# Kernel tuning notes

Measured on AMD Instinct MI355X. Metric: run time of the kernel, lower is better.

Reference implementation:

```python
import jax, jax.numpy as jnp
import numpy as np

N_NODES = 100000
N_EDGES = 1600000
IN_DIM, HIDDEN, OUT = 128, 64, 32


def setup_inputs() -> dict:
    key = jax.random.key(0)
    k1, k2, k3, k4 = jax.random.split(key, 4)
    x = jax.random.normal(k1, (N_NODES, IN_DIM), dtype=jnp.float32)
    edge_index = jax.random.randint(k2, (2, N_EDGES), 0, N_NODES, dtype=jnp.int64)
    # Glorot-style init for GCN weights
    W1 = jax.random.normal(k3, (IN_DIM, HIDDEN), dtype=jnp.float32) / np.sqrt(IN_DIM)
    b1 = jnp.zeros((HIDDEN,), dtype=jnp.float32)
    W2 = jax.random.normal(k4, (HIDDEN, OUT), dtype=jnp.float32) / np.sqrt(HIDDEN)
    b2 = jnp.zeros((OUT,), dtype=jnp.float32)
    return {"x": x, "edge_index": edge_index, "W1": W1, "b1": b1, "W2": W2, "b2": b2}


def _gcn_conv(x, src, dst, W, b, n_nodes):
    """PyG GCNConv: h = W x; symmetric-normalized scatter-add over edges
    (self-loops already appended to src/dst)."""
    h = x @ W  # [N, F_out] — transform first (F_out <= F_in)
    ones = jnp.ones_like(dst, dtype=h.dtype)
    deg = jax.ops.segment_sum(ones, dst, num_segments=n_nodes)  # in-degree incl. self-loop
    dinv = jnp.where(deg > 0, jax.lax.rsqrt(deg), 0.0)
    norm = dinv[src] * dinv[dst]  # [E]
    msg = h[src] * norm[:, None]  # [E, F_out] — dominant gather
    agg = jax.ops.segment_sum(msg, dst, num_segments=n_nodes)  # [N, F_out]
    return agg + b


def reference(x, edge_index, W1, b1, W2, b2):
    n_nodes = x.shape[0]
    loops = jnp.arange(n_nodes, dtype=edge_index.dtype)
    src = jnp.concatenate([edge_index[0], loops])
    dst = jnp.concatenate([edge_index[1], loops])
    h = jax.nn.relu(_gcn_conv(x, src, dst, W1, b1, n_nodes))
    out = jax.nn.relu(_gcn_conv(h, src, dst, W2, b2, n_nodes))
    return out
```

## Files before the change

### kernel.cpp

```cpp
#include <hip/hip_runtime.h>

#define IN_DIM 128
#define HID    64
#define OUTD   32

#define BSHIFT 9
#define BNODES 512
#define NB     196
#define BCAP   16384
#define CHUNK  4096

#define XPAD   136

typedef __attribute__((ext_vector_type(8))) short bf16x8;
typedef __attribute__((ext_vector_type(4))) float f32x4;


__device__ __forceinline__ unsigned bfp2(float x, float y) {
    unsigned a = __float_as_uint(x); a = a + 0x7FFF + ((a >> 16) & 1);
    unsigned b = __float_as_uint(y); b = b + 0x7FFF + ((b >> 16) & 1);
    return (a >> 16) | (b & 0xFFFF0000u);
}

__device__ __forceinline__ unsigned short bf1(float x) {
    unsigned u = __float_as_uint(x);
    u += 0x7FFF + ((u >> 16) & 1);
    return (unsigned short)(u >> 16);
}

__device__ __forceinline__ void acc8(float* f, uint4 q) {
    f[0] += __uint_as_float(q.x << 16); f[1] += __uint_as_float(q.x & 0xFFFF0000u);
    f[2] += __uint_as_float(q.y << 16); f[3] += __uint_as_float(q.y & 0xFFFF0000u);
    f[4] += __uint_as_float(q.z << 16); f[5] += __uint_as_float(q.z & 0xFFFF0000u);
    f[6] += __uint_as_float(q.w << 16); f[7] += __uint_as_float(q.w & 0xFFFF0000u);
}

__device__ __forceinline__ void facc8(float* f, uint4 q, float s) {
    f[0] = fmaf(__uint_as_float(q.x << 16),          s, f[0]);
    f[1] = fmaf(__uint_as_float(q.x & 0xFFFF0000u),  s, f[1]);
    f[2] = fmaf(__uint_as_float(q.y << 16),          s, f[2]);
    f[3] = fmaf(__uint_as_float(q.y & 0xFFFF0000u),  s, f[3]);
    f[4] = fmaf(__uint_as_float(q.z << 16),          s, f[4]);
    f[5] = fmaf(__uint_as_float(q.z & 0xFFFF0000u),  s, f[5]);
    f[6] = fmaf(__uint_as_float(q.w << 16),          s, f[6]);
    f[7] = fmaf(__uint_as_float(q.w & 0xFFFF0000u),  s, f[7]);
}


__launch_bounds__(256)
__global__ void k_bsct(const int* __restrict__ src, const int* __restrict__ dst,
                       int* __restrict__ bucketCursor, int* __restrict__ ebuf, int E) {
    __shared__ int h[NB];
    __shared__ int lbase[NB];
    __shared__ int lcur[NB];
    const int t = threadIdx.x;
    const int base = blockIdx.x * CHUNK;
    const int nI4 = (min(CHUNK, E - base)) >> 2;
    const int4* d4 = (const int4*)(dst + base);
    const int4* s4 = (const int4*)(src + base);

    int4 dv0, dv1, dv2, dv3;
    const bool v0 = t < nI4, v1 = t + 256 < nI4, v2 = t + 512 < nI4, v3 = t + 768 < nI4;
    if (v0) dv0 = d4[t];
    if (v1) dv1 = d4[t + 256];
    if (v2) dv2 = d4[t + 512];
    if (v3) dv3 = d4[t + 768];

    for (int i = t; i < NB; i += 256) { h[i] = 0; lcur[i] = 0; }
    __syncthreads();

    if (v0) { atomicAdd(&h[dv0.x >> BSHIFT], 1); atomicAdd(&h[dv0.y >> BSHIFT], 1);
              atomicAdd(&h[dv0.z >> BSHIFT], 1); atomicAdd(&h[dv0.w >> BSHIFT], 1); }
    if (v1) { atomicAdd(&h[dv1.x >> BSHIFT], 1); atomicAdd(&h[dv1.y >> BSHIFT], 1);
              atomicAdd(&h[dv1.z >> BSHIFT], 1); atomicAdd(&h[dv1.w >> BSHIFT], 1); }
    if (v2) { atomicAdd(&h[dv2.x >> BSHIFT], 1); atomicAdd(&h[dv2.y >> BSHIFT], 1);
              atomicAdd(&h[dv2.z >> BSHIFT], 1); atomicAdd(&h[dv2.w >> BSHIFT], 1); }
    if (v3) { atomicAdd(&h[dv3.x >> BSHIFT], 1); atomicAdd(&h[dv3.y >> BSHIFT], 1);
              atomicAdd(&h[dv3.z >> BSHIFT], 1); atomicAdd(&h[dv3.w >> BSHIFT], 1); }
    __syncthreads();

    for (int i = t; i < NB; i += 256)
        lbase[i] = h[i] ? atomicAdd(&bucketCursor[i], h[i]) : 0;
    __syncthreads();

    #define SC1(D, S) { int b_ = (D) >> BSHIFT; int off_ = atomicAdd(&lcur[b_], 1); \
                        ebuf[(size_t)b_ * BCAP + lbase[b_] + off_] = ((S) << BSHIFT) | ((D) & (BNODES - 1)); }
    if (v0) { int4 sv = s4[t];       SC1(dv0.x, sv.x); SC1(dv0.y, sv.y); SC1(dv0.z, sv.z); SC1(dv0.w, sv.w); }
    if (v1) { int4 sv = s4[t + 256]; SC1(dv1.x, sv.x); SC1(dv1.y, sv.y); SC1(dv1.z, sv.z); SC1(dv1.w, sv.w); }
    if (v2) { int4 sv = s4[t + 512]; SC1(dv2.x, sv.x); SC1(dv2.y, sv.y); SC1(dv2.z, sv.z); SC1(dv2.w, sv.w); }
    if (v3) { int4 sv = s4[t + 768]; SC1(dv3.x, sv.x); SC1(dv3.y, sv.y); SC1(dv3.z, sv.z); SC1(dv3.w, sv.w); }
    #undef SC1
}


__launch_bounds__(256)
__global__ void k_bfg(const int* __restrict__ ebuf, const int* __restrict__ bucketCursor,
                      int* __restrict__ rs, int* __restrict__ re, float* __restrict__ dinv,
                      int* __restrict__ csr,
                      const float* __restrict__ x, const float* __restrict__ W1,
                      unsigned short* __restrict__ hs1b, int N) {
    __shared__ int hist[BNODES];
    __shared__ int rsl[BNODES];
    __shared__ int ssum[256];
    __shared__ unsigned short xsb[64 * XPAD];
    __shared__ unsigned short wsb[64 * XPAD];
    const int t = threadIdx.x;

    if ((int)blockIdx.x < NB) {
        const int b = blockIdx.x;
        const int nodeBase = b << BSHIFT;
        const int ebase = b * BCAP;
        const int cnt = bucketCursor[b];
        const int nI4 = cnt >> 2;
        const int4* e4 = (const int4*)(ebuf + ebase);

        hist[t] = 0; hist[t + 256] = 0;
        __syncthreads();
        for (int i = t; i < nI4; i += 256) {
            int4 v = e4[i];
            atomicAdd(&hist[v.x & (BNODES - 1)], 1);
            atomicAdd(&hist[v.y & (BNODES - 1)], 1);
            atomicAdd(&hist[v.z & (BNODES - 1)], 1);
            atomicAdd(&hist[v.w & (BNODES - 1)], 1);
        }
        if (t < (cnt & 3))
            atomicAdd(&hist[ebuf[ebase + (nI4 << 2) + t] & (BNODES - 1)], 1);
        __syncthreads();

        int h0 = hist[2 * t], h1 = hist[2 * t + 1];
        ssum[t] = h0 + h1;
        __syncthreads();
        for (int off = 1; off < 256; off <<= 1) {
            int u = (t >= off) ? ssum[t - off] : 0;
            __syncthreads();
            ssum[t] += u;
            __syncthreads();
        }
        int excl = ssum[t] - h0 - h1;
        rsl[2 * t]     = excl;
        rsl[2 * t + 1] = excl + h0;

        int n0 = nodeBase + 2 * t, n1 = n0 + 1;
        if (n0 < N) {
            rs[n0] = ebase + excl;           re[n0] = ebase + excl + h0;
            dinv[n0] = rsqrtf((float)h0 + 1.0f);
        }
        if (n1 < N) {
            rs[n1] = ebase + excl + h0;      re[n1] = ebase + excl + h0 + h1;
            dinv[n1] = rsqrtf((float)h1 + 1.0f);
        }

        hist[2 * t] = 0; hist[2 * t + 1] = 0;
        __syncthreads();

        #define FILL1(P) { int l_ = (P) & (BNODES - 1); int off_ = atomicAdd(&hist[l_], 1); \
                           csr[ebase + rsl[l_] + off_] = ((unsigned)(P)) >> BSHIFT; }
        for (int i = t; i < nI4; i += 256) {
            int4 v = e4[i];
            FILL1(v.x); FILL1(v.y); FILL1(v.z); FILL1(v.w);
        }
        if (t < (cnt & 3))
            FILL1(ebuf[ebase + (nI4 << 2) + t]);
        #undef FILL1
    } else {
        const int base = ((int)blockIdx.x - NB) * 64;

        for (int i = t; i < IN_DIM * HID; i += 256) {
            int k = i >> 6, n = i & 63;
            wsb[n * XPAD + k] = bf1(W1[i]);
        }
        {
            const float4* s4 = (const float4*)(x + (size_t)base * IN_DIM);
            #pragma unroll
            for (int j = 0; j < 8; ++j) {
                int idx = t + j * 256;
                int r = idx >> 5, k4 = (idx & 31) * 4;
                ushort4 o;
                if (base + r < N) {
                    float4 v = s4[idx];
                    o.x = bf1(v.x); o.y = bf1(v.y); o.z = bf1(v.z); o.w = bf1(v.w);
                } else {
                    o.x = 0; o.y = 0; o.z = 0; o.w = 0;
                }
                *(ushort4*)&xsb[r * XPAD + k4] = o;
            }
        }
        __syncthreads();

        const int lane = t & 63;
        const int w    = t >> 6;
        const int lr   = lane & 15;
        const int kg   = lane >> 4;

        f32x4 acc0 = {0,0,0,0}, acc1 = {0,0,0,0}, acc2 = {0,0,0,0}, acc3 = {0,0,0,0};
        #pragma unroll
        for (int kb = 0; kb < 4; ++kb) {
            int ko = kb * 32 + kg * 8;
            bf16x8 af = *(const bf16x8*)&xsb[(w * 16 + lr) * XPAD + ko];
            bf16x8 b0 = *(const bf16x8*)&wsb[( 0 + lr) * XPAD + ko];
            bf16x8 b1 = *(const bf16x8*)&wsb[(16 + lr) * XPAD + ko];
            bf16x8 b2 = *(const bf16x8*)&wsb[(32 + lr) * XPAD + ko];
            bf16x8 b3 = *(const bf16x8*)&wsb[(48 + lr) * XPAD + ko];
            acc0 = __builtin_amdgcn_mfma_f32_16x16x32_bf16(af, b0, acc0, 0, 0, 0);
            acc1 = __builtin_amdgcn_mfma_f32_16x16x32_bf16(af, b1, acc1, 0, 0, 0);
            acc2 = __builtin_amdgcn_mfma_f32_16x16x32_bf16(af, b2, acc2, 0, 0, 0);
            acc3 = __builtin_amdgcn_mfma_f32_16x16x32_bf16(af, b3, acc3, 0, 0, 0);
        }

        #pragma unroll
        for (int j = 0; j < 4; ++j) {
            int node = base + w * 16 + kg * 4 + j;
            if (node < N) {
                unsigned short* o = hs1b + (size_t)node * HID + lr;
                o[0]  = bf1(acc0[j]);
                o[16] = bf1(acc1[j]);
                o[32] = bf1(acc2[j]);
                o[48] = bf1(acc3[j]);
            }
        }
    }
}


__launch_bounds__(128)
__global__ void k_fuse2(const uint4* __restrict__ hs, const int* __restrict__ rs,
                        const int* __restrict__ re, const int* __restrict__ csr,
                        const float* __restrict__ dinv,
                        const float* __restrict__ b1, const float* __restrict__ W2,
                        uint2* __restrict__ hs2b, int N) {
    __shared__ float Ws[HID * OUTD];
    __shared__ float L1s[16 * 68];
    const int t = threadIdx.x;
    const int base = blockIdx.x * 16;

    for (int i = t; i < HID * OUTD / 4; i += 128)
        ((float4*)Ws)[i] = ((const float4*)W2)[i];

    {
        int node = base + (t >> 3);
        int lane = t & 7;
        float dn = dinv[node];
        float fa[8] = {0,0,0,0,0,0,0,0};
        float fb[8] = {0,0,0,0,0,0,0,0};
        float fc[8] = {0,0,0,0,0,0,0,0};
        float fd[8] = {0,0,0,0,0,0,0,0};
        facc8(fa, hs[(size_t)node * 8 + lane], dn);
        int i = rs[node];
        const int end = re[node];
        for (; i + 4 <= end; i += 4) {
            int s0 = __builtin_nontemporal_load(csr + i);
            int s1 = __builtin_nontemporal_load(csr + i + 1);
            int s2 = __builtin_nontemporal_load(csr + i + 2);
            int s3 = __builtin_nontemporal_load(csr + i + 3);
            float d0 = dinv[s0], d1 = dinv[s1], d2 = dinv[s2], d3 = dinv[s3];
            uint4 q0 = hs[(size_t)s0 * 8 + lane];
            uint4 q1 = hs[(size_t)s1 * 8 + lane];
            uint4 q2 = hs[(size_t)s2 * 8 + lane];
            uint4 q3 = hs[(size_t)s3 * 8 + lane];
            facc8(fa, q0, d0); facc8(fb, q1, d1); facc8(fc, q2, d2); facc8(fd, q3, d3);
        }
        if (i + 2 <= end) {
            int s0 = __builtin_nontemporal_load(csr + i);
            int s1 = __builtin_nontemporal_load(csr + i + 1);
            float d0 = dinv[s0], d1 = dinv[s1];
            uint4 q0 = hs[(size_t)s0 * 8 + lane];
            uint4 q1 = hs[(size_t)s1 * 8 + lane];
            facc8(fa, q0, d0); facc8(fb, q1, d1);
            i += 2;
        }
        if (i < end) {
            int s0 = __builtin_nontemporal_load(csr + i);
            facc8(fa, hs[(size_t)s0 * 8 + lane], dinv[s0]);
        }
        const float4* bb4 = (const float4*)(b1 + lane * 8);
        float4 bv0 = bb4[0], bv1 = bb4[1];
        float* Lrow = &L1s[(t >> 3) * 68 + lane * 8];
        Lrow[0] = fmaxf((fa[0] + fb[0] + fc[0] + fd[0]) * dn + bv0.x, 0.0f);
        Lrow[1] = fmaxf((fa[1] + fb[1] + fc[1] + fd[1]) * dn + bv0.y, 0.0f);
        Lrow[2] = fmaxf((fa[2] + fb[2] + fc[2] + fd[2]) * dn + bv0.z, 0.0f);
        Lrow[3] = fmaxf((fa[3] + fb[3] + fc[3] + fd[3]) * dn + bv0.w, 0.0f);
        Lrow[4] = fmaxf((fa[4] + fb[4] + fc[4] + fd[4]) * dn + bv1.x, 0.0f);
        Lrow[5] = fmaxf((fa[5] + fb[5] + fc[5] + fd[5]) * dn + bv1.y, 0.0f);
        Lrow[6] = fmaxf((fa[6] + fb[6] + fc[6] + fd[6]) * dn + bv1.z, 0.0f);
        Lrow[7] = fmaxf((fa[7] + fb[7] + fc[7] + fd[7]) * dn + bv1.w, 0.0f);
    }
    __syncthreads();

    {
        const int fq = t & 7;
        const int nl = t >> 3;
        float4 a = {0,0,0,0};
        #pragma unroll 8
        for (int k = 0; k < HID; ++k) {
            float4 w = ((const float4*)Ws)[k * 8 + fq];
            float xv = L1s[nl * 68 + k];
            a.x += xv * w.x; a.y += xv * w.y; a.z += xv * w.z; a.w += xv * w.w;
        }
        int n = base + nl;
        float d = dinv[n];
        a.x *= d; a.y *= d; a.z *= d; a.w *= d;
        hs2b[(size_t)n * 8 + fq] = make_uint2(bfp2(a.x, a.y), bfp2(a.z, a.w));
    }
}


__launch_bounds__(128)
__global__ void k_agg2(const uint4* __restrict__ hs, const int* __restrict__ rs,
                       const int* __restrict__ re, const int* __restrict__ csr,
                       const float* __restrict__ dinv,
                       const float* __restrict__ b2, float* __restrict__ out, int N) {
    int tid = blockIdx.x * 128 + threadIdx.x;
    int node = tid >> 2;
    int lane = tid & 3;

    float fa[8] = {0,0,0,0,0,0,0,0};
    float fb[8] = {0,0,0,0,0,0,0,0};
    float fc[8] = {0,0,0,0,0,0,0,0};
    float fd[8] = {0,0,0,0,0,0,0,0};
    acc8(fa, hs[(size_t)node * 4 + lane]);
    int i = rs[node];
    const int end = re[node];
    for (; i + 4 <= end; i += 4) {
        int s0 = __builtin_nontemporal_load(csr + i);
        int s1 = __builtin_nontemporal_load(csr + i + 1);
        int s2 = __builtin_nontemporal_load(csr + i + 2);
        int s3 = __builtin_nontemporal_load(csr + i + 3);
        uint4 q0 = hs[(size_t)s0 * 4 + lane];
        uint4 q1 = hs[(size_t)s1 * 4 + lane];
        uint4 q2 = hs[(size_t)s2 * 4 + lane];
        uint4 q3 = hs[(size_t)s3 * 4 + lane];
        acc8(fa, q0); acc8(fb, q1); acc8(fc, q2); acc8(fd, q3);
    }
    if (i + 2 <= end) {
        int s0 = __builtin_nontemporal_load(csr + i);
        int s1 = __builtin_nontemporal_load(csr + i + 1);
        uint4 q0 = hs[(size_t)s0 * 4 + lane];
        uint4 q1 = hs[(size_t)s1 * 4 + lane];
        acc8(fa, q0); acc8(fb, q1);
        i += 2;
    }
    if (i < end) {
        int s0 = __builtin_nontemporal_load(csr + i);
        acc8(fa, hs[(size_t)s0 * 4 + lane]);
    }
    float dn = dinv[node];
    const float4* bb4 = (const float4*)(b2 + lane * 8);
    float4 b0 = bb4[0], b1v = bb4[1];
    float4 o0, o1;
    o0.x = fmaxf((fa[0] + fb[0] + fc[0] + fd[0]) * dn + b0.x, 0.0f);
    o0.y = fmaxf((fa[1] + fb[1] + fc[1] + fd[1]) * dn + b0.y, 0.0f);
    o0.z = fmaxf((fa[2] + fb[2] + fc[2] + fd[2]) * dn + b0.z, 0.0f);
    o0.w = fmaxf((fa[3] + fb[3] + fc[3] + fd[3]) * dn + b0.w, 0.0f);
    o1.x = fmaxf((fa[4] + fb[4] + fc[4] + fd[4]) * dn + b1v.x, 0.0f);
    o1.y = fmaxf((fa[5] + fb[5] + fc[5] + fd[5]) * dn + b1v.y, 0.0f);
    o1.z = fmaxf((fa[6] + fb[6] + fc[6] + fd[6]) * dn + b1v.z, 0.0f);
    o1.w = fmaxf((fa[7] + fb[7] + fc[7] + fd[7]) * dn + b1v.w, 0.0f);
    float4* o = (float4*)(out + (size_t)node * OUTD + lane * 8);
    o[0] = o0;
    o[1] = o1;
}


extern "C" void kernel_launch(void* const* d_in, const int* in_sizes, int n_in,
                              void* d_out, int out_size, void* d_ws, size_t ws_size,
                              hipStream_t stream) {
    const float* x  = (const float*)d_in[0];
    const int*   ei = (const int*)  d_in[1];
    const float* W1 = (const float*)d_in[2];
    const float* b1 = (const float*)d_in[3];
    const float* W2 = (const float*)d_in[4];
    const float* b2 = (const float*)d_in[5];

    const int N = in_sizes[0] / IN_DIM;
    const int E = in_sizes[1] / 2;
    const int* srcI = ei;
    const int* dstI = ei + E;
    float* out = (float*)d_out;

    float* dinv         = (float*)d_ws;
    int*   rs           = (int*)d_ws + 131072;
    int*   re           = (int*)d_ws + 2 * 131072;
    int*   bucketCursor = (int*)d_ws + 3 * 131072;
    int*   ebuf         = (int*)d_ws + 4 * 131072;
    int*   csr          = ebuf + (size_t)NB * BCAP;
    uint2* hs1b         = (uint2*)(csr + (size_t)NB * BCAP);
    uint2* hs2b         = hs1b + (size_t)N * 16;

    const int nBsc = (E + CHUNK - 1) / CHUNK;
    const int nG1  = (N + 63) / 64;

    hipMemsetAsync(bucketCursor, 0, NB * sizeof(int), stream);
    k_bsct <<<nBsc, 256, 0, stream>>>(srcI, dstI, bucketCursor, ebuf, E);
    k_bfg  <<<NB + nG1, 256, 0, stream>>>(ebuf, bucketCursor, rs, re, dinv, csr,
                                          x, W1, (unsigned short*)hs1b, N);
    k_fuse2<<<N / 16, 128, 0, stream>>>((const uint4*)hs1b, rs, re, csr, dinv, b1, W2, hs2b, N);
    k_agg2 <<<N / 32, 128, 0, stream>>>((const uint4*)hs2b, rs, re, csr, dinv, b2, out, N);
}
```

Measured before the change: 123.7 us.

## Replace global bucket cursors with per-chunk fixed-capacity bucket segments

Result: faster. 117.6 us, median of 2 (-4.9%).

```diff
diff --git a/kernel.cpp b/kernel.cpp
--- a/kernel.cpp
+++ b/kernel.cpp
@@ -9,6 +9,7 @@
 #define NB     196
 #define BCAP   16384
 #define CHUNK  4096
+#define SEGCAP 64
 
 #define XPAD   136
 
@@ -49,9 +50,8 @@
 
 __launch_bounds__(256)
 __global__ void k_bsct(const int* __restrict__ src, const int* __restrict__ dst,
-                       int* __restrict__ bucketCursor, int* __restrict__ ebuf, int E) {
+                       int* __restrict__ counts, int* __restrict__ ebuf, int E) {
     __shared__ int h[NB];
-    __shared__ int lbase[NB];
     __shared__ int lcur[NB];
     const int t = threadIdx.x;
     const int base = blockIdx.x * CHUNK;
@@ -80,11 +80,11 @@
     __syncthreads();
 
     for (int i = t; i < NB; i += 256)
-        lbase[i] = h[i] ? atomicAdd(&bucketCursor[i], h[i]) : 0;
-    __syncthreads();
-
+        counts[(size_t)blockIdx.x * NB + i] = h[i];
+
+    const size_t segBase = (size_t)blockIdx.x * NB * SEGCAP;
     #define SC1(D, S) { int b_ = (D) >> BSHIFT; int off_ = atomicAdd(&lcur[b_], 1); \
-                        ebuf[(size_t)b_ * BCAP + lbase[b_] + off_] = ((S) << BSHIFT) | ((D) & (BNODES - 1)); }
+                        ebuf[segBase + (size_t)b_ * SEGCAP + off_] = ((S) << BSHIFT) | ((D) & (BNODES - 1)); }
     if (v0) { int4 sv = s4[t];       SC1(dv0.x, sv.x); SC1(dv0.y, sv.y); SC1(dv0.z, sv.z); SC1(dv0.w, sv.w); }
     if (v1) { int4 sv = s4[t + 256]; SC1(dv1.x, sv.x); SC1(dv1.y, sv.y); SC1(dv1.z, sv.z); SC1(dv1.w, sv.w); }
     if (v2) { int4 sv = s4[t + 512]; SC1(dv2.x, sv.x); SC1(dv2.y, sv.y); SC1(dv2.z, sv.z); SC1(dv2.w, sv.w); }
@@ -94,9 +94,9 @@
 
 
 __launch_bounds__(256)
-__global__ void k_bfg(const int* __restrict__ ebuf, const int* __restrict__ bucketCursor,
+__global__ void k_bfg(const int* __restrict__ ebuf, const int* __restrict__ counts,
                       int* __restrict__ rs, int* __restrict__ re, float* __restrict__ dinv,
-                      int* __restrict__ csr,
+                      int* __restrict__ csr, int nChunks,
                       const float* __restrict__ x, const float* __restrict__ W1,
                       unsigned short* __restrict__ hs1b, int N) {
     __shared__ int hist[BNODES];
@@ -110,21 +110,15 @@
         const int b = blockIdx.x;
         const int nodeBase = b << BSHIFT;
         const int ebase = b * BCAP;
-        const int cnt = bucketCursor[b];
-        const int nI4 = cnt >> 2;
-        const int4* e4 = (const int4*)(ebuf + ebase);
 
         hist[t] = 0; hist[t + 256] = 0;
         __syncthreads();
-        for (int i = t; i < nI4; i += 256) {
-            int4 v = e4[i];
-            atomicAdd(&hist[v.x & (BNODES - 1)], 1);
-            atomicAdd(&hist[v.y & (BNODES - 1)], 1);
-            atomicAdd(&hist[v.z & (BNODES - 1)], 1);
-            atomicAdd(&hist[v.w & (BNODES - 1)], 1);
-        }
-        if (t < (cnt & 3))
-            atomicAdd(&hist[ebuf[ebase + (nI4 << 2) + t] & (BNODES - 1)], 1);
+        for (int c = t; c < nChunks; c += 256) {
+            int cnt = counts[(size_t)c * NB + b];
+            const int* seg = ebuf + ((size_t)c * NB + b) * SEGCAP;
+            for (int j = 0; j < cnt; ++j)
+                atomicAdd(&hist[seg[j] & (BNODES - 1)], 1);
+        }
         __syncthreads();
 
         int h0 = hist[2 * t], h1 = hist[2 * t + 1];
@@ -153,15 +147,16 @@
         hist[2 * t] = 0; hist[2 * t + 1] = 0;
         __syncthreads();
 
-        #define FILL1(P) { int l_ = (P) & (BNODES - 1); int off_ = atomicAdd(&hist[l_], 1); \
-                           csr[ebase + rsl[l_] + off_] = ((unsigned)(P)) >> BSHIFT; }
-        for (int i = t; i < nI4; i += 256) {
-            int4 v = e4[i];
-            FILL1(v.x); FILL1(v.y); FILL1(v.z); FILL1(v.w);
-        }
-        if (t < (cnt & 3))
-            FILL1(ebuf[ebase + (nI4 << 2) + t]);
-        #undef FILL1
+        for (int c = t; c < nChunks; c += 256) {
+            int cnt = counts[(size_t)c * NB + b];
+            const int* seg = ebuf + ((size_t)c * NB + b) * SEGCAP;
+            for (int j = 0; j < cnt; ++j) {
+                int p = seg[j];
+                int l = p & (BNODES - 1);
+                int off = atomicAdd(&hist[l], 1);
+                csr[ebase + rsl[l] + off] = ((unsigned)p) >> BSHIFT;
+            }
+        }
     } else {
         const int base = ((int)blockIdx.x - NB) * 64;
 
@@ -377,21 +372,20 @@
     const int* dstI = ei + E;
     float* out = (float*)d_out;
 
-    float* dinv         = (float*)d_ws;
-    int*   rs           = (int*)d_ws + 131072;
-    int*   re           = (int*)d_ws + 2 * 131072;
-    int*   bucketCursor = (int*)d_ws + 3 * 131072;
-    int*   ebuf         = (int*)d_ws + 4 * 131072;
-    int*   csr          = ebuf + (size_t)NB * BCAP;
-    uint2* hs1b         = (uint2*)(csr + (size_t)NB * BCAP);
-    uint2* hs2b         = hs1b + (size_t)N * 16;
-
-    const int nBsc = (E + CHUNK - 1) / CHUNK;
-    const int nG1  = (N + 63) / 64;
-
-    hipMemsetAsync(bucketCursor, 0, NB * sizeof(int), stream);
-    k_bsct <<<nBsc, 256, 0, stream>>>(srcI, dstI, bucketCursor, ebuf, E);
-    k_bfg  <<<NB + nG1, 256, 0, stream>>>(ebuf, bucketCursor, rs, re, dinv, csr,
+    const int nChunks = (E + CHUNK - 1) / CHUNK;
+    const int nG1     = (N + 63) / 64;
+
+    float* dinv   = (float*)d_ws;
+    int*   rs     = (int*)d_ws + 131072;
+    int*   re     = (int*)d_ws + 2 * 131072;
+    int*   counts = (int*)d_ws + 3 * 131072;
+    int*   ebuf   = (int*)d_ws + 4 * 131072;
+    int*   csr    = ebuf + (size_t)nChunks * NB * SEGCAP;
+    uint2* hs1b   = (uint2*)(csr + (size_t)NB * BCAP);
+    uint2* hs2b   = hs1b + (size_t)N * 16;
+
+    k_bsct <<<nChunks, 256, 0, stream>>>(srcI, dstI, counts, ebuf, E);
+    k_bfg  <<<NB + nG1, 256, 0, stream>>>(ebuf, counts, rs, re, dinv, csr, nChunks,
                                           x, W1, (unsigned short*)hs1b, N);
     k_fuse2<<<N / 16, 128, 0, stream>>>((const uint4*)hs1b, rs, re, csr, dinv, b1, W2, hs2b, N);
     k_agg2 <<<N / 32, 128, 0, stream>>>((const uint4*)hs2b, rs, re, csr, dinv, b2, out, N);
```
